# Kernel tuning notes

Hardware: AMD Instinct MI355X
Metric: run time of the kernel (lower is better)

The kernel has to match this reference:

```python
import jax, jax.numpy as jnp
import numpy as np
from jax import lax

NDIMS = 3
NUM_SCALES = 3
WINDOW_SIZE = 9
POOL_K = 3


def box_filter(x, win):
    """Separable mean (box) filter, kernel=ones/win^3, same padding. x: [N,C,D,H,W]."""
    pad = win // 2
    for ax in range(NDIMS):
        kshape = [1, 1] + [1] * NDIMS
        kshape[2 + ax] = win
        k = jnp.ones(kshape, x.dtype) / win
        padding = [(pad, pad) if i == ax else (0, 0) for i in range(NDIMS)]
        x = lax.conv_general_dilated(x, k, window_strides=(1,) * NDIMS,
                                     padding=padding,
                                     dimension_numbers=('NCDHW', 'OIDHW', 'NCDHW'))
    return x


def avg_pool3d(x, k=POOL_K, stride=2):
    """avg_pool3d with count_include_pad=False."""
    pad = k // 2
    window = (1, 1, k, k, k)
    strides = (1, 1, stride, stride, stride)
    padding = ((0, 0), (0, 0), (pad, pad), (pad, pad), (pad, pad))
    s = lax.reduce_window(x, jnp.array(0, x.dtype), lax.add, window, strides, padding)
    cnt = lax.reduce_window(jnp.ones_like(x), jnp.array(0, x.dtype), lax.add,
                            window, strides, padding)
    return s / cnt


def single_scale_ncc(Ii, Ji, win):
    mu1 = box_filter(Ii, win)
    mu2 = box_filter(Ji, win)
    sigma1_sq = box_filter(Ii * Ii, win) - mu1 * mu1
    sigma2_sq = box_filter(Ji * Ji, win) - mu2 * mu2
    sigma12 = box_filter(Ii * Ji, win) - mu1 * mu2
    eps = jnp.finfo(sigma12.dtype).eps
    cc = sigma12 * sigma12 / jnp.maximum(sigma1_sq * sigma2_sq, eps)
    return -jnp.mean(cc)


def setup_inputs() -> dict:
    key = jax.random.key(0)
    k1, k2 = jax.random.split(key)
    shape = (2, 1, 160, 192, 160)
    I = jax.random.uniform(k1, shape, dtype=jnp.float32)
    J = jax.random.uniform(k2, shape, dtype=jnp.float32)
    return {"I": I, "J": J}


def reference(I, J):
    # Multi-scale NCC: losses at windows 9/7/5 on pyramid built by stride-2 avg pooling.
    total = jnp.zeros((), I.dtype)
    for i in range(NUM_SCALES):
        # SingleScaleNCC(pred=I, target=J): Ii=target, Ji=pred (symmetric metric)
        total = total + single_scale_ncc(J, I, WINDOW_SIZE - 2 * i) / NUM_SCALES
        if i < NUM_SCALES - 1:
            I = avg_pool3d(I)
            J = avg_pool3d(J)
    return total
```

## Files before the change

kernel.cpp:

```cpp
#include <hip/hip_runtime.h>

#define NCC_EPS 1.1920929e-07f

template<int WIN>
__global__ __launch_bounds__(256)
void ncc_pad_kernel(const float* __restrict__ Pi, const float* __restrict__ Pj,
                    int Dp, int Hp, int Wp, int Dreal, int Wreal,
                    int tilesH, int tilesW, int chunksD, int chunkLen,
                    double* __restrict__ acc)
{
    constexpr int RAD  = WIN / 2;
    constexpr int TH = 16, TW = 16;
    constexpr int WROWS = TH + 2 * RAD;
    constexpr int PSTR = 68;
    constexpr int QSTR = 24;
    constexpr int OFF  = 4 - RAD;
    constexpr int NWT  = WROWS * 4;
    constexpr float invV = 1.0f / (float)(WIN * WIN * WIN);

    __shared__ __align__(16) float wb0123[2][WROWS * PSTR];
    __shared__ __align__(16) float wb4[2][WROWS * QSTR];
    __shared__ float red[4];

    int bid = blockIdx.x;
    int tw = bid % tilesW; bid /= tilesW;
    int th = bid % tilesH; bid /= tilesH;
    int cd = bid % chunksD; bid /= chunksD;
    int b  = bid;

    const int h0 = th * TH, w0 = tw * TW;
    const int z0 = cd * chunkLen;
    const int z1 = min(z0 + chunkLen, Dreal);

    const size_t plane = (size_t)Hp * Wp;
    const float* Ib = Pi + (size_t)b * Dp * plane;
    const float* Jb = Pj + (size_t)b * Dp * plane;

    const int t  = threadIdx.x;
    const int hh = t >> 4, ww = t & 15;
    const bool valid = (w0 + ww) < Wreal;

    const int wr  = t >> 2;
    const int wc4 = t & 3;
    const bool wact = t < NWT;
    const size_t rowoff = (size_t)(h0 + wr) * Wp + (w0 + 4 * wc4);

    auto load_slice = [&](int zp, float (&fi)[12], float (&fj)[12]) {
        if (wact) {
            const float* rI = Ib + (size_t)zp * plane + rowoff;
            const float* rJ = Jb + (size_t)zp * plane + rowoff;
            float4 a0 = *reinterpret_cast<const float4*>(rI);
            float4 a1 = *reinterpret_cast<const float4*>(rI + 4);
            float4 a2 = *reinterpret_cast<const float4*>(rI + 8);
            float4 b0 = *reinterpret_cast<const float4*>(rJ);
            float4 b1 = *reinterpret_cast<const float4*>(rJ + 4);
            float4 b2 = *reinterpret_cast<const float4*>(rJ + 8);
            fi[0]=a0.x; fi[1]=a0.y; fi[2]=a0.z; fi[3]=a0.w;
            fi[4]=a1.x; fi[5]=a1.y; fi[6]=a1.z; fi[7]=a1.w;
            fi[8]=a2.x; fi[9]=a2.y; fi[10]=a2.z; fi[11]=a2.w;
            fj[0]=b0.x; fj[1]=b0.y; fj[2]=b0.z; fj[3]=b0.w;
            fj[4]=b1.x; fj[5]=b1.y; fj[6]=b1.z; fj[7]=b1.w;
            fj[8]=b2.x; fj[9]=b2.y; fj[10]=b2.z; fj[11]=b2.w;
        }
    };

    float ring[WIN][5];
    float rs[5];
    #pragma unroll
    for (int s = 0; s < WIN; ++s)
        #pragma unroll
        for (int c = 0; c < 5; ++c) ring[s][c] = 0.f;
    #pragma unroll
    for (int c = 0; c < 5; ++c) rs[c] = 0.f;

    float ccsum = 0.f;

    float fiC[12], fjC[12], fiN[12], fjN[12];
    const int zend = z1 + RAD;
    load_slice(z0 - RAD + 4, fiC, fjC);

    for (int zb = z0 - RAD; zb < zend; zb += WIN) {
        #pragma unroll
        for (int ph = 0; ph < WIN; ++ph) {
            const int z = zb + ph;
            if (z < zend) {
                const int zpn = min(z + 5, Dp - 1);
                load_slice(zpn, fiN, fjN);

                const int par = (z + 4) & 1;
                float n0, n1, n2, n3, n4;
                if (wact) {
                    float s0 = 0, s1 = 0, s2 = 0, s3 = 0, s4 = 0;
                    #pragma unroll
                    for (int k = 0; k < WIN; ++k) {
                        float a = fiC[OFF + k], bb = fjC[OFF + k];
                        s0 += a; s1 += bb;
                        s2 = fmaf(a, a, s2);
                        s3 = fmaf(bb, bb, s3);
                        s4 = fmaf(a, bb, s4);
                    }
                    float o0[4], o1[4], o2[4], o3[4], o4[4];
                    o0[0]=s0; o1[0]=s1; o2[0]=s2; o3[0]=s3; o4[0]=s4;
                    #pragma unroll
                    for (int m = 1; m < 4; ++m) {
                        float aL = fiC[OFF + m - 1],       bL = fjC[OFF + m - 1];
                        float aR = fiC[OFF + m - 1 + WIN], bR = fjC[OFF + m - 1 + WIN];
                        s0 += aR - aL;
                        s1 += bR - bL;
                        s2 = s2 + aR * aR - aL * aL;
                        s3 = s3 + bR * bR - bL * bL;
                        s4 = s4 + aR * bR - aL * bL;
                        o0[m]=s0; o1[m]=s1; o2[m]=s2; o3[m]=s3; o4[m]=s4;
                    }
                    #pragma unroll
                    for (int m = 0; m < 4; ++m) {
                        *reinterpret_cast<float4*>(&wb0123[par][wr * PSTR + 16 * wc4 + 4 * m]) =
                            make_float4(o0[m], o1[m], o2[m], o3[m]);
                    }
                    *reinterpret_cast<float4*>(&wb4[par][wr * QSTR + 4 * wc4]) =
                        make_float4(o4[0], o4[1], o4[2], o4[3]);
                }
                __builtin_amdgcn_sched_barrier(0);
                asm volatile("s_waitcnt lgkmcnt(0)");
                __builtin_amdgcn_s_barrier();
                __builtin_amdgcn_sched_barrier(0);
                {
                    float4 a4 = make_float4(0.f, 0.f, 0.f, 0.f);
                    float nn4 = 0.f;
                    #pragma unroll
                    for (int dh = 0; dh < WIN; ++dh) {
                        float4 v = *reinterpret_cast<const float4*>(
                            &wb0123[par][(hh + dh) * PSTR + 4 * ww]);
                        a4.x += v.x; a4.y += v.y; a4.z += v.z; a4.w += v.w;
                        nn4 += wb4[par][(hh + dh) * QSTR + ww];
                    }
                    n0 = a4.x; n1 = a4.y; n2 = a4.z; n3 = a4.w; n4 = nn4;
                }
                rs[0] += n0 - ring[ph][0]; ring[ph][0] = n0;
                rs[1] += n1 - ring[ph][1]; ring[ph][1] = n1;
                rs[2] += n2 - ring[ph][2]; ring[ph][2] = n2;
                rs[3] += n3 - ring[ph][3]; ring[ph][3] = n3;
                rs[4] += n4 - ring[ph][4]; ring[ph][4] = n4;

                const int zo = z - RAD;
                if (valid && zo >= z0) {
                    float muI = rs[0] * invV;
                    float muJ = rs[1] * invV;
                    float sII = rs[2] * invV - muI * muI;
                    float sJJ = rs[3] * invV - muJ * muJ;
                    float s12 = rs[4] * invV - muI * muJ;
                    float cc = (s12 * s12) / fmaxf(sII * sJJ, NCC_EPS);
                    ccsum += cc;
                }
                #pragma unroll
                for (int e = 0; e < 12; ++e) { fiC[e] = fiN[e]; fjC[e] = fjN[e]; }
            }
        }
    }

    for (int off = 32; off > 0; off >>= 1)
        ccsum += __shfl_down(ccsum, off);
    const int wid = t >> 6, lane = t & 63;
    if (lane == 0) red[wid] = ccsum;
    __syncthreads();
    if (t == 0) {
        float s = red[0] + red[1] + red[2] + red[3];
        atomicAdd(acc, (double)s);
    }
}

__global__ void pad_kernel(const float* __restrict__ inA, const float* __restrict__ inB,
                           float* __restrict__ outA, float* __restrict__ outB,
                           int D, int H, int W, int Dp, int Hp, int Wp, int nchunks)
{
    int idx = blockIdx.x * 256 + threadIdx.x;
    if (idx >= 2 * nchunks) return;
    const bool isB = idx >= nchunks;
    int k = isB ? idx - nchunks : idx;
    const float* in = isB ? inB : inA;
    float* out = isB ? outB : outA;
    const int WC = Wp / 4;
    int wc = k % WC; int tmp = k / WC;
    int hp = tmp % Hp; tmp /= Hp;
    int zp = tmp % Dp; int b = tmp / Dp;
    int z = zp - 4, h = hp - 4, w0 = 4 * wc - 4;
    float4 v = make_float4(0.f, 0.f, 0.f, 0.f);
    if (z >= 0 && z < D && h >= 0 && h < H && w0 >= 0 && w0 + 4 <= W)
        v = *reinterpret_cast<const float4*>(in + ((size_t)(b * D + z) * H + h) * W + w0);
    *reinterpret_cast<float4*>(out + ((size_t)(b * Dp + zp) * Hp + hp) * Wp + 4 * wc) = v;
}

__global__ void pool_pad_kernel(const float* __restrict__ inA, const float* __restrict__ inB,
                                float* __restrict__ outA, float* __restrict__ outB,
                                int D, int H, int W, int iDp, int iHp, int iWp,
                                int oD, int oH, int oW, int oDp, int oHp, int oWp,
                                int total)
{
    int idx0 = blockIdx.x * 256 + threadIdx.x;
    if (idx0 >= 2 * total) return;
    const bool isB = idx0 >= total;
    int idx = isB ? idx0 - total : idx0;
    const float* in = isB ? inB : inA;
    float* out = isB ? outB : outA;

    int ow = idx % oW; int tmp = idx / oW;
    int oh = tmp % oH; tmp /= oH;
    int od = tmp % oD; int b = tmp / oD;

    const size_t ip = (size_t)iHp * iWp;
    const float* ib = in + (size_t)b * iDp * ip;
    float s = 0.f;
    #pragma unroll
    for (int dd = 0; dd < 3; ++dd)
        #pragma unroll
        for (int dh = 0; dh < 3; ++dh) {
            const float* r = ib + (size_t)(2 * od + 3 + dd) * ip
                                + (size_t)(2 * oh + 3 + dh) * iWp + (2 * ow + 3);
            s += r[0] + r[1] + r[2];
        }
    int dlo = max(2 * od - 1, 0), dhi = min(2 * od + 2, D);
    int hlo = max(2 * oh - 1, 0), hhi = min(2 * oh + 2, H);
    int wlo = max(2 * ow - 1, 0), whi = min(2 * ow + 2, W);
    int cnt = (dhi - dlo) * (hhi - hlo) * (whi - wlo);
    out[((size_t)(b * oDp + od + 4) * oHp + (oh + 4)) * oWp + (ow + 4)] = s / (float)cnt;
}

template<int WIN>
__global__ __launch_bounds__(256)
void ncc_scale_kernel(const float* __restrict__ I, const float* __restrict__ J,
                      int D, int H, int W,
                      int tilesH, int tilesW, int chunksD, int chunkLen,
                      double* __restrict__ acc)
{
    constexpr int RAD  = WIN / 2;
    constexpr int TH = 16, TW = 16;
    constexpr int WROWS = TH + 2 * RAD;
    constexpr int PSTR = 68;
    constexpr int QSTR = 24;
    constexpr int OFF  = 4 - RAD;
    constexpr int NWT  = WROWS * 4;
    constexpr float invV = 1.0f / (float)(WIN * WIN * WIN);

    __shared__ __align__(16) float wb0123[2][WROWS * PSTR];
    __shared__ __align__(16) float wb4[2][WROWS * QSTR];
    __shared__ float red[4];

    int bid = blockIdx.x;
    int tw = bid % tilesW; bid /= tilesW;
    int th = bid % tilesH; bid /= tilesH;
    int cd = bid % chunksD; bid /= chunksD;
    int b  = bid;

    const int h0 = th * TH, w0 = tw * TW;
    const int z0 = cd * chunkLen;
    const int z1 = min(z0 + chunkLen, D);

    const size_t plane = (size_t)H * W;
    const float* Ib = I + (size_t)b * D * plane;
    const float* Jb = J + (size_t)b * D * plane;

    const int t  = threadIdx.x;
    const int hh = t >> 4, ww = t & 15;
    const int gh = h0 + hh, gw = w0 + ww;
    const bool valid = (gh < H) && (gw < W);

    const int wr  = t >> 2;
    const int wc4 = t & 3;
    const bool wact = t < NWT;
    const int wbase = w0 + 4 * wc4 - 4;
    const int wghr  = h0 + wr - RAD;

    auto load_slice = [&](int z, float (&fi)[12], float (&fj)[12]) {
        const bool zok = (z >= 0) && (z < D);
        if (zok && wact && wghr >= 0 && wghr < H) {
            const float* rowI = Ib + (size_t)z * plane + (size_t)wghr * W;
            const float* rowJ = Jb + (size_t)z * plane + (size_t)wghr * W;
            if (wbase >= 0 && wbase + 12 <= W) {
                float4 a0 = *reinterpret_cast<const float4*>(rowI + wbase);
                float4 a1 = *reinterpret_cast<const float4*>(rowI + wbase + 4);
                float4 a2 = *reinterpret_cast<const float4*>(rowI + wbase + 8);
                float4 b0 = *reinterpret_cast<const float4*>(rowJ + wbase);
                float4 b1 = *reinterpret_cast<const float4*>(rowJ + wbase + 4);
                float4 b2 = *reinterpret_cast<const float4*>(rowJ + wbase + 8);
                fi[0]=a0.x; fi[1]=a0.y; fi[2]=a0.z; fi[3]=a0.w;
                fi[4]=a1.x; fi[5]=a1.y; fi[6]=a1.z; fi[7]=a1.w;
                fi[8]=a2.x; fi[9]=a2.y; fi[10]=a2.z; fi[11]=a2.w;
                fj[0]=b0.x; fj[1]=b0.y; fj[2]=b0.z; fj[3]=b0.w;
                fj[4]=b1.x; fj[5]=b1.y; fj[6]=b1.z; fj[7]=b1.w;
                fj[8]=b2.x; fj[9]=b2.y; fj[10]=b2.z; fj[11]=b2.w;
            } else {
                #pragma unroll
                for (int e = 0; e < 12; ++e) {
                    int cg = wbase + e;
                    bool ok = (cg >= 0) && (cg < W);
                    fi[e] = ok ? rowI[cg] : 0.f;
                    fj[e] = ok ? rowJ[cg] : 0.f;
                }
            }
        } else {
            #pragma unroll
            for (int e = 0; e < 12; ++e) { fi[e] = 0.f; fj[e] = 0.f; }
        }
    };

    float ring[WIN][5];
    float rs[5];
    #pragma unroll
    for (int s = 0; s < WIN; ++s)
        #pragma unroll
        for (int c = 0; c < 5; ++c) ring[s][c] = 0.f;
    #pragma unroll
    for (int c = 0; c < 5; ++c) rs[c] = 0.f;

    float ccsum = 0.f;

    float fiC[12], fjC[12], fiN[12], fjN[12];
    const int zend = z1 + RAD;
    load_slice(z0 - RAD, fiC, fjC);

    for (int zb = z0 - RAD; zb < zend; zb += WIN) {
        #pragma unroll
        for (int ph = 0; ph < WIN; ++ph) {
            const int z = zb + ph;
            if (z < zend) {
                const bool zin = (z >= 0) && (z < D);
                load_slice((z + 1 < zend) ? z + 1 : -1, fiN, fjN);
                float n0 = 0, n1 = 0, n2 = 0, n3 = 0, n4 = 0;
                if (zin) {
                    const int par = (z + 64) & 1;
                    if (wact) {
                        float s0 = 0, s1 = 0, s2 = 0, s3 = 0, s4 = 0;
                        #pragma unroll
                        for (int k = 0; k < WIN; ++k) {
                            float a = fiC[OFF + k], bb = fjC[OFF + k];
                            s0 += a; s1 += bb;
                            s2 = fmaf(a, a, s2);
                            s3 = fmaf(bb, bb, s3);
                            s4 = fmaf(a, bb, s4);
                        }
                        float o0[4], o1[4], o2[4], o3[4], o4[4];
                        o0[0]=s0; o1[0]=s1; o2[0]=s2; o3[0]=s3; o4[0]=s4;
                        #pragma unroll
                        for (int m = 1; m < 4; ++m) {
                            float aL = fiC[OFF + m - 1],       bL = fjC[OFF + m - 1];
                            float aR = fiC[OFF + m - 1 + WIN], bR = fjC[OFF + m - 1 + WIN];
                            s0 += aR - aL;
                            s1 += bR - bL;
                            s2 = s2 + aR * aR - aL * aL;
                            s3 = s3 + bR * bR - bL * bL;
                            s4 = s4 + aR * bR - aL * bL;
                            o0[m]=s0; o1[m]=s1; o2[m]=s2; o3[m]=s3; o4[m]=s4;
                        }
                        #pragma unroll
                        for (int m = 0; m < 4; ++m) {
                            *reinterpret_cast<float4*>(&wb0123[par][wr * PSTR + 16 * wc4 + 4 * m]) =
                                make_float4(o0[m], o1[m], o2[m], o3[m]);
                        }
                        *reinterpret_cast<float4*>(&wb4[par][wr * QSTR + 4 * wc4]) =
                            make_float4(o4[0], o4[1], o4[2], o4[3]);
                    }
                    __syncthreads();
                    float4 a4 = make_float4(0.f, 0.f, 0.f, 0.f);
                    #pragma unroll
                    for (int dh = 0; dh < WIN; ++dh) {
                        float4 v = *reinterpret_cast<const float4*>(
                            &wb0123[par][(hh + dh) * PSTR + 4 * ww]);
                        a4.x += v.x; a4.y += v.y; a4.z += v.z; a4.w += v.w;
                        n4 += wb4[par][(hh + dh) * QSTR + ww];
                    }
                    n0 = a4.x; n1 = a4.y; n2 = a4.z; n3 = a4.w;
                }
                rs[0] += n0 - ring[ph][0]; ring[ph][0] = n0;
                rs[1] += n1 - ring[ph][1]; ring[ph][1] = n1;
                rs[2] += n2 - ring[ph][2]; ring[ph][2] = n2;
                rs[3] += n3 - ring[ph][3]; ring[ph][3] = n3;
                rs[4] += n4 - ring[ph][4]; ring[ph][4] = n4;

                const int zo = z - RAD;
                if (valid && zo >= z0) {
                    float muI = rs[0] * invV;
                    float muJ = rs[1] * invV;
                    float sII = rs[2] * invV - muI * muI;
                    float sJJ = rs[3] * invV - muJ * muJ;
                    float s12 = rs[4] * invV - muI * muJ;
                    float cc = (s12 * s12) / fmaxf(sII * sJJ, NCC_EPS);
                    ccsum += cc;
                }
                #pragma unroll
                for (int e = 0; e < 12; ++e) { fiC[e] = fiN[e]; fjC[e] = fjN[e]; }
            }
        }
    }

    for (int off = 32; off > 0; off >>= 1)
        ccsum += __shfl_down(ccsum, off);
    const int wid = t >> 6, lane = t & 63;
    if (lane == 0) red[wid] = ccsum;
    __syncthreads();
    if (t == 0) {
        float s = red[0] + red[1] + red[2] + red[3];
        atomicAdd(acc, (double)s);
    }
}

__global__ void pool_kernel2(const float* __restrict__ inA, const float* __restrict__ inB,
                             float* __restrict__ outA, float* __restrict__ outB,
                             int D, int H, int W, int oD, int oH, int oW, int total)
{
    int idx0 = blockIdx.x * 256 + threadIdx.x;
    if (idx0 >= 2 * total) return;
    const bool isB = idx0 >= total;
    int idx = isB ? idx0 - total : idx0;
    const float* in = isB ? inB : inA;
    float* out = isB ? outB : outA;

    int ow = idx % oW; int tmp = idx / oW;
    int oh = tmp % oH; tmp /= oH;
    int od = tmp % oD; int b = tmp / oD;

    int d0 = 2 * od - 1, h0 = 2 * oh - 1, w0 = 2 * ow - 1;
    int dlo = max(d0, 0), dhi = min(d0 + 3, D);
    int hlo = max(h0, 0), hhi = min(h0 + 3, H);
    int wlo = max(w0, 0), whi = min(w0 + 3, W);

    const float* ib = in + (size_t)b * D * H * W;
    float s = 0.f;
    for (int d = dlo; d < dhi; ++d)
        for (int h = hlo; h < hhi; ++h)
            for (int w = wlo; w < whi; ++w)
                s += ib[((size_t)d * H + h) * W + w];
    int cnt = (dhi - dlo) * (hhi - hlo) * (whi - wlo);
    out[idx] = s / (float)cnt;
}

__global__ void finalize_kernel(const double* __restrict__ acc, float* __restrict__ out)
{
    double m = acc[0] / 9830400.0 + acc[1] / 1228800.0 + acc[2] / 153600.0;
    out[0] = (float)(-m / 3.0);
}

extern "C" void kernel_launch(void* const* d_in, const int* in_sizes, int n_in,
                              void* d_out, int out_size, void* d_ws, size_t ws_size,
                              hipStream_t stream)
{
    const float* I0 = (const float*)d_in[0];
    const float* J0 = (const float*)d_in[1];
    float* out = (float*)d_out;

    char* ws = (char*)d_ws;
    double* acc = (double*)ws;
    hipMemsetAsync(acc, 0, 3 * sizeof(double), stream);

    const size_t P0SZ = (size_t)2 * 168 * 200 * 168;
    const size_t P1SZ = (size_t)2 * 88 * 104 * 88;
    const size_t P2SZ = (size_t)2 * 48 * 56 * 56;
    const size_t need_pad = 256 + (2 * P0SZ + 2 * P1SZ + 2 * P2SZ) * sizeof(float);

    if (ws_size >= need_pad) {
        float* P0I = (float*)(ws + 256);
        float* P0J = P0I + P0SZ;
        float* P1I = P0J + P0SZ;
        float* P1J = P1I + P1SZ;
        float* P2I = P1J + P1SZ;
        float* P2J = P2I + P2SZ;

        hipMemsetAsync(P1I, 0, (2 * P1SZ + 2 * P2SZ) * sizeof(float), stream);

        {
            int nchunks = (int)(P0SZ / 4);
            int blocks = (2 * nchunks + 255) / 256;
            pad_kernel<<<blocks, 256, 0, stream>>>(I0, J0, P0I, P0J,
                                                   160, 192, 160, 168, 200, 168, nchunks);
        }
        ncc_pad_kernel<9><<<2 * 12 * 10 * 4, 256, 0, stream>>>(
            P0I, P0J, 168, 200, 168, 160, 160, 12, 10, 4, 40, acc + 0);
        {
            int total = 2 * 80 * 96 * 80;
            int blocks = (2 * total + 255) / 256;
            pool_pad_kernel<<<blocks, 256, 0, stream>>>(P0I, P0J, P1I, P1J,
                                                        160, 192, 160, 168, 200, 168,
                                                        80, 96, 80, 88, 104, 88, total);
        }
        ncc_pad_kernel<7><<<2 * 6 * 5 * 4, 256, 0, stream>>>(
            P1I, P1J, 88, 104, 88, 80, 80, 6, 5, 4, 20, acc + 1);
        {
            int total = 2 * 40 * 48 * 40;
            int blocks = (2 * total + 255) / 256;
            pool_pad_kernel<<<blocks, 256, 0, stream>>>(P1I, P1J, P2I, P2J,
                                                        80, 96, 80, 88, 104, 88,
                                                        40, 48, 40, 48, 56, 56, total);
        }
        ncc_pad_kernel<5><<<2 * 3 * 3 * 5, 256, 0, stream>>>(
            P2I, P2J, 48, 56, 56, 40, 40, 3, 3, 5, 8, acc + 2);
    } else {
        float* I1 = (float*)(ws + 256);
        float* J1 = I1 + (size_t)2 * 80 * 96 * 80;
        float* I2 = J1 + (size_t)2 * 80 * 96 * 80;
        float* J2 = I2 + (size_t)2 * 40 * 48 * 40;

        ncc_scale_kernel<9><<<2 * 12 * 10 * 4, 256, 0, stream>>>(
            I0, J0, 160, 192, 160, 12, 10, 4, 40, acc + 0);
        {
            int total = 2 * 80 * 96 * 80;
            int blocks = (2 * total + 255) / 256;
            pool_kernel2<<<blocks, 256, 0, stream>>>(I0, J0, I1, J1,
                                                     160, 192, 160, 80, 96, 80, total);
        }
        ncc_scale_kernel<7><<<2 * 6 * 5 * 8, 256, 0, stream>>>(
            I1, J1, 80, 96, 80, 6, 5, 8, 10, acc + 1);
        {
            int total = 2 * 40 * 48 * 40;
            int blocks = (2 * total + 255) / 256;
            pool_kernel2<<<blocks, 256, 0, stream>>>(I1, J1, I2, J2,
                                                     80, 96, 80, 40, 48, 40, total);
        }
        ncc_scale_kernel<5><<<2 * 3 * 3 * 14, 256, 0, stream>>>(
            I2, J2, 40, 48, 40, 3, 3, 14, 3, acc + 2);
    }

    finalize_kernel<<<1, 1, 0, stream>>>(acc, out);
}
```

Measured before the change: 190.5 us.

## Replace full scale-0 padding with small edge strips and direct pooling

Removes the full padded copy of both scale-0 volumes. In its place, a small kernel copies the left and right 16-wide W edge strips into side buffers. The scale-0 NCC kernel reads interior tiles straight from the original inputs, reads edge tiles from the strips, and points out-of-range rows and slices at a zero buffer. The first pooling now reads the unpadded inputs with bounds-checked loops. This avoids writing and re-reading roughly 80 MB of padded data, at the cost of per-thread pointer selection and less regular pooling loads.

```diff
diff --git a/kernel.cpp b/kernel.cpp
--- a/kernel.cpp
+++ b/kernel.cpp
@@ -1,6 +1,214 @@
 #include <hip/hip_runtime.h>
 
 #define NCC_EPS 1.1920929e-07f
+
+template<int WIN>
+__global__ __launch_bounds__(256)
+void ncc_strip_kernel(const float* __restrict__ I, const float* __restrict__ J,
+                      const float* __restrict__ SLI, const float* __restrict__ SRI,
+                      const float* __restrict__ SLJ, const float* __restrict__ SRJ,
+                      const float* __restrict__ zerobuf,
+                      int D, int H, int W,
+                      int tilesH, int tilesW, int chunksD, int chunkLen,
+                      double* __restrict__ acc)
+{
+    constexpr int RAD  = WIN / 2;
+    constexpr int TH = 16, TW = 16;
+    constexpr int WROWS = TH + 2 * RAD;
+    constexpr int PSTR = 68;
+    constexpr int QSTR = 24;
+    constexpr int OFF  = 4 - RAD;
+    constexpr int NWT  = WROWS * 4;
+    constexpr float invV = 1.0f / (float)(WIN * WIN * WIN);
+
+    __shared__ __align__(16) float wb0123[2][WROWS * PSTR];
+    __shared__ __align__(16) float wb4[2][WROWS * QSTR];
+    __shared__ float red[4];
+
+    int bid = blockIdx.x;
+    int tw = bid % tilesW; bid /= tilesW;
+    int th = bid % tilesH; bid /= tilesH;
+    int cd = bid % chunksD; bid /= chunksD;
+    int b  = bid;
+
+    const int h0 = th * TH, w0 = tw * TW;
+    const int z0 = cd * chunkLen;
+    const int z1 = min(z0 + chunkLen, D);
+
+    const size_t plane = (size_t)H * W;
+
+    const int t  = threadIdx.x;
+    const int hh = t >> 4, ww = t & 15;
+    const bool valid = (w0 + ww) < W;
+
+    const int wr  = t >> 2;
+    const int wc4 = t & 3;
+    const bool wact = t < NWT;
+    const int wbase = w0 + 4 * wc4 - 4;
+    const int wghr  = h0 + wr - RAD;
+
+    const float *bI, *bJ;
+    long pstr;
+    const bool rowOOB = (wghr < 0) || (wghr >= H);
+    if (!wact || rowOOB) {
+        bI = zerobuf; bJ = zerobuf; pstr = 0;
+    } else if (wbase < 0) {
+        size_t off = ((size_t)b * D * H + (size_t)wghr) * 16 + (wbase + 4);
+        bI = SLI + off; bJ = SLJ + off; pstr = (long)H * 16;
+    } else if (wbase + 12 > W) {
+        size_t off = ((size_t)b * D * H + (size_t)wghr) * 16 + (wbase - (W - 12));
+        bI = SRI + off; bJ = SRJ + off; pstr = (long)H * 16;
+    } else {
+        size_t off = (size_t)b * D * plane + (size_t)wghr * W + wbase;
+        bI = I + off; bJ = J + off; pstr = (long)plane;
+    }
+
+    auto load_slice = [&](int z, float (&fi)[12], float (&fj)[12]) {
+        if (wact) {
+            const bool zok = (z >= 0) && (z < D);
+            const float* pI = zok ? (bI + (size_t)((long)z * pstr)) : zerobuf;
+            const float* pJ = zok ? (bJ + (size_t)((long)z * pstr)) : zerobuf;
+            float4 a0 = *reinterpret_cast<const float4*>(pI);
+            float4 a1 = *reinterpret_cast<const float4*>(pI + 4);
+            float4 a2 = *reinterpret_cast<const float4*>(pI + 8);
+            float4 b0 = *reinterpret_cast<const float4*>(pJ);
+            float4 b1 = *reinterpret_cast<const float4*>(pJ + 4);
+            float4 b2 = *reinterpret_cast<const float4*>(pJ + 8);
+            fi[0]=a0.x; fi[1]=a0.y; fi[2]=a0.z; fi[3]=a0.w;
+            fi[4]=a1.x; fi[5]=a1.y; fi[6]=a1.z; fi[7]=a1.w;
+            fi[8]=a2.x; fi[9]=a2.y; fi[10]=a2.z; fi[11]=a2.w;
+            fj[0]=b0.x; fj[1]=b0.y; fj[2]=b0.z; fj[3]=b0.w;
+            fj[4]=b1.x; fj[5]=b1.y; fj[6]=b1.z; fj[7]=b1.w;
+            fj[8]=b2.x; fj[9]=b2.y; fj[10]=b2.z; fj[11]=b2.w;
+        }
+    };
+
+    float ring[WIN][5];
+    float rs[5];
+    #pragma unroll
+    for (int s = 0; s < WIN; ++s)
+        #pragma unroll
+        for (int c = 0; c < 5; ++c) ring[s][c] = 0.f;
+    #pragma unroll
+    for (int c = 0; c < 5; ++c) rs[c] = 0.f;
+
+    float ccsum = 0.f;
+
+    float fiC[12], fjC[12], fiN[12], fjN[12];
+    const int zend = z1 + RAD;
+    load_slice(z0 - RAD, fiC, fjC);
+
+    for (int zb = z0 - RAD; zb < zend; zb += WIN) {
+        #pragma unroll
+        for (int ph = 0; ph < WIN; ++ph) {
+            const int z = zb + ph;
+            if (z < zend) {
+                load_slice(z + 1, fiN, fjN);
+
+                const int par = (z + 8) & 1;
+                float n0, n1, n2, n3, n4;
+                if (wact) {
+                    float s0 = 0, s1 = 0, s2 = 0, s3 = 0, s4 = 0;
+                    #pragma unroll
+                    for (int k = 0; k < WIN; ++k) {
+                        float a = fiC[OFF + k], bb = fjC[OFF + k];
+                        s0 += a; s1 += bb;
+                        s2 = fmaf(a, a, s2);
+                        s3 = fmaf(bb, bb, s3);
+                        s4 = fmaf(a, bb, s4);
+                    }
+                    float o0[4], o1[4], o2[4], o3[4], o4[4];
+                    o0[0]=s0; o1[0]=s1; o2[0]=s2; o3[0]=s3; o4[0]=s4;
+                    #pragma unroll
+                    for (int m = 1; m < 4; ++m) {
+                        float aL = fiC[OFF + m - 1],       bL = fjC[OFF + m - 1];
+                        float aR = fiC[OFF + m - 1 + WIN], bR = fjC[OFF + m - 1 + WIN];
+                        s0 += aR - aL;
+                        s1 += bR - bL;
+                        s2 = s2 + aR * aR - aL * aL;
+                        s3 = s3 + bR * bR - bL * bL;
+                        s4 = s4 + aR * bR - aL * bL;
+                        o0[m]=s0; o1[m]=s1; o2[m]=s2; o3[m]=s3; o4[m]=s4;
+                    }
+                    #pragma unroll
+                    for (int m = 0; m < 4; ++m) {
+                        *reinterpret_cast<float4*>(&wb0123[par][wr * PSTR + 16 * wc4 + 4 * m]) =
+                            make_float4(o0[m], o1[m], o2[m], o3[m]);
+                    }
+                    *reinterpret_cast<float4*>(&wb4[par][wr * QSTR + 4 * wc4]) =
+                        make_float4(o4[0], o4[1], o4[2], o4[3]);
+                }
+                __builtin_amdgcn_sched_barrier(0);
+                asm volatile("s_waitcnt lgkmcnt(0)");
+                __builtin_amdgcn_s_barrier();
+                __builtin_amdgcn_sched_barrier(0);
+                {
+                    float4 a4 = make_float4(0.f, 0.f, 0.f, 0.f);
+                    float nn4 = 0.f;
+                    #pragma unroll
+                    for (int dh = 0; dh < WIN; ++dh) {
+                        float4 v = *reinterpret_cast<const float4*>(
+                            &wb0123[par][(hh + dh) * PSTR + 4 * ww]);
+                        a4.x += v.x; a4.y += v.y; a4.z += v.z; a4.w += v.w;
+                        nn4 += wb4[par][(hh + dh) * QSTR + ww];
+                    }
+                    n0 = a4.x; n1 = a4.y; n2 = a4.z; n3 = a4.w; n4 = nn4;
+                }
+                rs[0] += n0 - ring[ph][0]; ring[ph][0] = n0;
+                rs[1] += n1 - ring[ph][1]; ring[ph][1] = n1;
+                rs[2] += n2 - ring[ph][2]; ring[ph][2] = n2;
+                rs[3] += n3 - ring[ph][3]; ring[ph][3] = n3;
+                rs[4] += n4 - ring[ph][4]; ring[ph][4] = n4;
+
+                const int zo = z - RAD;
+                if (valid && zo >= z0) {
+                    float muI = rs[0] * invV;
+                    float muJ = rs[1] * invV;
+                    float sII = rs[2] * invV - muI * muI;
+                    float sJJ = rs[3] * invV - muJ * muJ;
+                    float s12 = rs[4] * invV - muI * muJ;
+                    float cc = (s12 * s12) / fmaxf(sII * sJJ, NCC_EPS);
+                    ccsum += cc;
+                }
+                #pragma unroll
+                for (int e = 0; e < 12; ++e) { fiC[e] = fiN[e]; fjC[e] = fjN[e]; }
+            }
+        }
+    }
+
+    for (int off = 32; off > 0; off >>= 1)
+        ccsum += __shfl_down(ccsum, off);
+    const int wid = t >> 6, lane = t & 63;
+    if (lane == 0) red[wid] = ccsum;
+    __syncthreads();
+    if (t == 0) {
+        float s = red[0] + red[1] + red[2] + red[3];
+        atomicAdd(acc, (double)s);
+    }
+}
+
+__global__ void strip_fill(const float* __restrict__ I, const float* __restrict__ J,
+                           float* __restrict__ SLI, float* __restrict__ SRI,
+                           float* __restrict__ SLJ, float* __restrict__ SRJ,
+                           int D, int H, int W, int N1)
+{
+    int idx = blockIdx.x * 256 + threadIdx.x;
+    if (idx >= 4 * N1) return;
+    int bufid = idx / N1;
+    int r = idx - bufid * N1;
+    int c4 = r & 3; r >>= 2;
+    int h = r % H; int zb = r / H;
+
+    const float* in = (bufid >= 2) ? J : I;
+    float* out = (bufid == 0) ? SLI : (bufid == 1) ? SRI : (bufid == 2) ? SLJ : SRJ;
+    const bool right = bufid & 1;
+    const int c0 = 4 * c4 + (right ? (W - 12) : -4);
+
+    float4 v = make_float4(0.f, 0.f, 0.f, 0.f);
+    if (c0 >= 0 && c0 + 4 <= W)
+        v = *reinterpret_cast<const float4*>(in + ((size_t)zb * H + h) * W + c0);
+    *reinterpret_cast<float4*>(out + ((size_t)zb * H + h) * 16 + 4 * c4) = v;
+}
 
 template<int WIN>
 __global__ __launch_bounds__(256)
@@ -169,25 +377,34 @@
     }
 }
 
-__global__ void pad_kernel(const float* __restrict__ inA, const float* __restrict__ inB,
-                           float* __restrict__ outA, float* __restrict__ outB,
-                           int D, int H, int W, int Dp, int Hp, int Wp, int nchunks)
-{
-    int idx = blockIdx.x * 256 + threadIdx.x;
-    if (idx >= 2 * nchunks) return;
-    const bool isB = idx >= nchunks;
-    int k = isB ? idx - nchunks : idx;
+__global__ void pool_b2p_kernel(const float* __restrict__ inA, const float* __restrict__ inB,
+                                float* __restrict__ outA, float* __restrict__ outB,
+                                int D, int H, int W, int oD, int oH, int oW,
+                                int oDp, int oHp, int oWp, int total)
+{
+    int idx0 = blockIdx.x * 256 + threadIdx.x;
+    if (idx0 >= 2 * total) return;
+    const bool isB = idx0 >= total;
+    int idx = isB ? idx0 - total : idx0;
     const float* in = isB ? inB : inA;
     float* out = isB ? outB : outA;
-    const int WC = Wp / 4;
-    int wc = k % WC; int tmp = k / WC;
-    int hp = tmp % Hp; tmp /= Hp;
-    int zp = tmp % Dp; int b = tmp / Dp;
-    int z = zp - 4, h = hp - 4, w0 = 4 * wc - 4;
-    float4 v = make_float4(0.f, 0.f, 0.f, 0.f);
-    if (z >= 0 && z < D && h >= 0 && h < H && w0 >= 0 && w0 + 4 <= W)
-        v = *reinterpret_cast<const float4*>(in + ((size_t)(b * D + z) * H + h) * W + w0);
-    *reinterpret_cast<float4*>(out + ((size_t)(b * Dp + zp) * Hp + hp) * Wp + 4 * wc) = v;
+
+    int ow = idx % oW; int tmp = idx / oW;
+    int oh = tmp % oH; tmp /= oH;
+    int od = tmp % oD; int b = tmp / oD;
+
+    int dlo = max(2 * od - 1, 0), dhi = min(2 * od + 2, D);
+    int hlo = max(2 * oh - 1, 0), hhi = min(2 * oh + 2, H);
+    int wlo = max(2 * ow - 1, 0), whi = min(2 * ow + 2, W);
+
+    const float* ib = in + (size_t)b * D * H * W;
+    float s = 0.f;
+    for (int d = dlo; d < dhi; ++d)
+        for (int h = hlo; h < hhi; ++h)
+            for (int w = wlo; w < whi; ++w)
+                s += ib[((size_t)d * H + h) * W + w];
+    int cnt = (dhi - dlo) * (hhi - hlo) * (whi - wlo);
+    out[((size_t)(b * oDp + od + 4) * oHp + (oh + 4)) * oWp + (ow + 4)] = s / (float)cnt;
 }
 
 __global__ void pool_pad_kernel(const float* __restrict__ inA, const float* __restrict__ inB,
@@ -216,7 +433,7 @@
         for (int dh = 0; dh < 3; ++dh) {
             const float* r = ib + (size_t)(2 * od + 3 + dd) * ip
                                 + (size_t)(2 * oh + 3 + dh) * iWp + (2 * ow + 3);
-            s += r[0] + r[1] + r[2];
+            s += r[0]; s += r[1]; s += r[2];
         }
     int dlo = max(2 * od - 1, 0), dhi = min(2 * od + 2, D);
     int hlo = max(2 * oh - 1, 0), hhi = min(2 * oh + 2, H);
@@ -418,10 +635,9 @@
     int oh = tmp % oH; tmp /= oH;
     int od = tmp % oD; int b = tmp / oD;
 
-    int d0 = 2 * od - 1, h0 = 2 * oh - 1, w0 = 2 * ow - 1;
-    int dlo = max(d0, 0), dhi = min(d0 + 3, D);
-    int hlo = max(h0, 0), hhi = min(h0 + 3, H);
-    int wlo = max(w0, 0), whi = min(w0 + 3, W);
+    int dlo = max(2 * od - 1, 0), dhi = min(2 * od + 2, D);
+    int hlo = max(2 * oh - 1, 0), hhi = min(2 * oh + 2, H);
+    int wlo = max(2 * ow - 1, 0), whi = min(2 * ow + 2, W);
 
     const float* ib = in + (size_t)b * D * H * W;
     float s = 0.f;
@@ -448,38 +664,42 @@
     float* out = (float*)d_out;
 
     char* ws = (char*)d_ws;
-    double* acc = (double*)ws;
-    hipMemsetAsync(acc, 0, 3 * sizeof(double), stream);
-
-    const size_t P0SZ = (size_t)2 * 168 * 200 * 168;
+    float* zerobuf = (float*)ws;
+    double* acc = (double*)(ws + 192);
+
+    const size_t SSZ  = (size_t)2 * 160 * 192 * 16;
     const size_t P1SZ = (size_t)2 * 88 * 104 * 88;
     const size_t P2SZ = (size_t)2 * 48 * 56 * 56;
-    const size_t need_pad = 256 + (2 * P0SZ + 2 * P1SZ + 2 * P2SZ) * sizeof(float);
-
-    if (ws_size >= need_pad) {
-        float* P0I = (float*)(ws + 256);
-        float* P0J = P0I + P0SZ;
-        float* P1I = P0J + P0SZ;
+    const size_t need = 256 + (4 * SSZ + 2 * P1SZ + 2 * P2SZ) * sizeof(float);
+
+    if (ws_size >= need) {
+        float* SLI = (float*)(ws + 256);
+        float* SRI = SLI + SSZ;
+        float* SLJ = SRI + SSZ;
+        float* SRJ = SLJ + SSZ;
+        float* P1I = SRJ + SSZ;
         float* P1J = P1I + P1SZ;
         float* P2I = P1J + P1SZ;
         float* P2J = P2I + P2SZ;
 
+        hipMemsetAsync(ws, 0, 256, stream);
         hipMemsetAsync(P1I, 0, (2 * P1SZ + 2 * P2SZ) * sizeof(float), stream);
 
         {
-            int nchunks = (int)(P0SZ / 4);
-            int blocks = (2 * nchunks + 255) / 256;
-            pad_kernel<<<blocks, 256, 0, stream>>>(I0, J0, P0I, P0J,
-                                                   160, 192, 160, 168, 200, 168, nchunks);
-        }
-        ncc_pad_kernel<9><<<2 * 12 * 10 * 4, 256, 0, stream>>>(
-            P0I, P0J, 168, 200, 168, 160, 160, 12, 10, 4, 40, acc + 0);
+            int N1 = 2 * 160 * 192 * 4;
+            int blocks = (4 * N1 + 255) / 256;
+            strip_fill<<<blocks, 256, 0, stream>>>(I0, J0, SLI, SRI, SLJ, SRJ,
+                                                   160, 192, 160, N1);
+        }
+        ncc_strip_kernel<9><<<2 * 12 * 10 * 4, 256, 0, stream>>>(
+            I0, J0, SLI, SRI, SLJ, SRJ, zerobuf,
+            160, 192, 160, 12, 10, 4, 40, acc + 0);
         {
             int total = 2 * 80 * 96 * 80;
             int blocks = (2 * total + 255) / 256;
-            pool_pad_kernel<<<blocks, 256, 0, stream>>>(P0I, P0J, P1I, P1J,
-                                                        160, 192, 160, 168, 200, 168,
-                                                        80, 96, 80, 88, 104, 88, total);
+            pool_b2p_kernel<<<blocks, 256, 0, stream>>>(I0, J0, P1I, P1J,
+                                                        160, 192, 160, 80, 96, 80,
+                                                        88, 104, 88, total);
         }
         ncc_pad_kernel<7><<<2 * 6 * 5 * 4, 256, 0, stream>>>(
             P1I, P1J, 88, 104, 88, 80, 80, 6, 5, 4, 20, acc + 1);
@@ -493,6 +713,7 @@
         ncc_pad_kernel<5><<<2 * 3 * 3 * 5, 256, 0, stream>>>(
             P2I, P2J, 48, 56, 56, 40, 40, 3, 3, 5, 8, acc + 2);
     } else {
+        hipMemsetAsync(ws, 0, 256, stream);
         float* I1 = (float*)(ws + 256);
         float* J1 = I1 + (size_t)2 * 80 * 96 * 80;
         float* I2 = J1 + (size_t)2 * 80 * 96 * 80;
```

New measurement: 201.8 us. 6.0% more time.
